# Performance work log

Measured on AMD Instinct MI355X. Metric: run time of the kernel, lower is better.

The kernel has to match this reference:

```python
import math
import jax, jax.numpy as jnp
import numpy as np

D_IN, R_S, T_MAX = 1024, 256, 2048
B, T = 8, 2048


def setup_inputs() -> dict:
    key = jax.random.key(0)
    ks = jax.random.split(key, 8)
    u = jax.random.normal(ks[0], (B, T, D_IN), dtype=jnp.float32)
    h0_r = jax.random.normal(ks[1], (B, R_S), dtype=jnp.float32)
    h0_i = jax.random.normal(ks[2], (B, R_S), dtype=jnp.float32)
    # parameters (lambda_raw randomized instead of zeros so sigmoid is nontrivial)
    lambda_raw = jax.random.normal(ks[3], (R_S,), dtype=jnp.float32)
    # omega init exactly as in the torch module
    log_min, log_max = math.log(1.0 / T_MAX), math.log(math.pi)
    n = np.arange(1, R_S + 1, dtype=np.float32)
    weyl_freqs = n * math.pi / R_S
    log_freqs = np.exp(np.linspace(log_min, log_max, R_S, dtype=np.float32))
    omega = jnp.asarray(0.5 * weyl_freqs + 0.5 * log_freqs, dtype=jnp.float32)
    W_proj = jax.random.normal(ks[4], (R_S, D_IN), dtype=jnp.float32) / math.sqrt(D_IN)
    W_res = jax.random.normal(ks[5], (2 * R_S, D_IN), dtype=jnp.float32) / math.sqrt(D_IN)
    ln_gamma = jnp.ones((2 * R_S,), dtype=jnp.float32)
    ln_beta = jnp.zeros((2 * R_S,), dtype=jnp.float32)
    return {"u": u, "h0_r": h0_r, "h0_i": h0_i, "lambda_raw": lambda_raw,
            "omega": omega, "W_proj": W_proj, "W_res": W_res,
            "ln_gamma": ln_gamma, "ln_beta": ln_beta}


def _layernorm(x, gamma, beta, eps=1e-5):
    mu = jnp.mean(x, axis=-1, keepdims=True)
    var = jnp.mean(jnp.square(x - mu), axis=-1, keepdims=True)
    return (x - mu) * jax.lax.rsqrt(var + eps) * gamma + beta


def reference(u, h0_r, h0_i, lambda_raw, omega, W_proj, W_res, ln_gamma, ln_beta):
    Bb, Tt, _ = u.shape
    lam = -jax.nn.sigmoid(lambda_raw) * 5.0                      # [R]
    t = jnp.arange(Tt, dtype=jnp.float32)                        # [T]
    decay = jnp.exp(lam[:, None] * t[None, :])                   # [R,T]
    phase = omega[:, None] * t[None, :]                          # [R,T]
    f_r = decay * jnp.cos(phase)
    f_i = decay * jnp.sin(phase)
    u_proj = jnp.einsum('btd,rd->brt', u, W_proj)                # [B,R,T]
    n_fft = 2 * Tt
    U_f = jnp.fft.rfft(u_proj, n=n_fft, axis=-1)                 # [B,R,F]
    F_r = jnp.fft.rfft(f_r, n=n_fft, axis=-1)[None]              # [1,R,F]
    F_i = jnp.fft.rfft(f_i, n=n_fft, axis=-1)[None]
    h_r = jnp.fft.irfft(U_f * F_r, n=n_fft, axis=-1)[..., :Tt]   # [B,R,T]
    h_i = jnp.fft.irfft(U_f * F_i, n=n_fft, axis=-1)[..., :Tt]
    # ZIR correction from initial state
    t_zir = t + 1.0
    decay_z = jnp.exp(lam[:, None] * t_zir[None, :])             # [R,T]
    phase_z = omega[:, None] * t_zir[None, :]
    f_r_z = decay_z * jnp.cos(phase_z)
    f_i_z = decay_z * jnp.sin(phase_z)
    h0r = h0_r[:, :, None]                                       # [B,R,1]
    h0i = h0_i[:, :, None]
    h_r = h_r + h0r * f_r_z[None] - h0i * f_i_z[None]
    h_i = h_i + h0r * f_i_z[None] + h0i * f_r_z[None]
    h_r = jnp.swapaxes(h_r, 1, 2)                                # [B,T,R]
    h_i = jnp.swapaxes(h_i, 1, 2)
    ssm_out = jnp.concatenate([h_r, h_i], axis=-1)               # [B,T,2R]
    res = jnp.einsum('btd,ed->bte', u, W_res)                    # [B,T,2R]
    out = _layernorm(ssm_out + res, ln_gamma, ln_beta)
    final_r = jax.lax.stop_gradient(h_r[:, -1])
    final_i = jax.lax.stop_gradient(h_i[:, -1])
    return out, final_r, final_i
```

## Files before the change

### kernel.cpp

```cpp
#include <hip/hip_runtime.h>
#include <math.h>

#define T_LEN 2048
#define BB    8
#define RS    256
#define DIN   1024
#define NE    768
#define M_TOT (BB * T_LEN)
#define LCH   32
#define NCH   (T_LEN / LCH)
#define OUT_MAIN (M_TOT * 512)

typedef unsigned short ushort;
typedef unsigned int   uint;
typedef short  short8  __attribute__((ext_vector_type(8)));
typedef float  f32x4   __attribute__((ext_vector_type(4)));
typedef ushort ushort8 __attribute__((ext_vector_type(8)));

__device__ __forceinline__ ushort f2bf_rn(float x) {
    uint u = __float_as_uint(x);
    return (ushort)((u + 0x7FFFu + ((u >> 16) & 1u)) >> 16);
}
__device__ __forceinline__ float bf2f(ushort b) {
    return __uint_as_float(((uint)b) << 16);
}

__device__ __forceinline__ void gload16(const ushort* g, ushort* l) {
    __builtin_amdgcn_global_load_lds(
        (const __attribute__((address_space(1))) uint*)g,
        (__attribute__((address_space(3))) uint*)l, 16, 0, 0);
}

#define N8U  (M_TOT * DIN / 8)
#define N8WP (RS * DIN / 8)
#define N8WR (2 * RS * DIN / 8)
#define N8TOT (N8U + N8WP + N8WR)

__global__ __launch_bounds__(256) void split_kernel(
    const float* __restrict__ u, const float* __restrict__ wp,
    const float* __restrict__ wr, ushort* __restrict__ Uhi,
    ushort* __restrict__ Ulo, ushort* __restrict__ Whi, ushort* __restrict__ Wlo)
{
    const int i = blockIdx.x * 256 + threadIdx.x;
    if (i >= N8TOT) return;
    const float* src; ushort* hi; ushort* lo; int j;
    if (i < N8U)              { src = u;  hi = Uhi; lo = Ulo; j = i; }
    else if (i < N8U + N8WP)  { src = wp; hi = Whi; lo = Wlo; j = i - N8U; }
    else                      { src = wr; hi = Whi + (size_t)RS * DIN;
                                lo = Wlo + (size_t)RS * DIN; j = i - N8U - N8WP; }
    const float4 x0 = ((const float4*)src)[(size_t)j * 2 + 0];
    const float4 x1 = ((const float4*)src)[(size_t)j * 2 + 1];
    const float xs[8] = {x0.x, x0.y, x0.z, x0.w, x1.x, x1.y, x1.z, x1.w};
    ushort8 hv, lv;
#pragma unroll
    for (int k = 0; k < 8; ++k) {
        const ushort hb = f2bf_rn(xs[k]);
        hv[k] = hb;
        lv[k] = f2bf_rn(xs[k] - bf2f(hb));
    }
    ((ushort8*)hi)[j] = hv;
    ((ushort8*)lo)[j] = lv;
}

#define Bb 128
#define BK 32

__global__ __launch_bounds__(256) void gemm_mfma(
    const ushort* __restrict__ Uh, const ushort* __restrict__ Ul,
    const ushort* __restrict__ Wh, const ushort* __restrict__ Wl,
    float* __restrict__ C)
{
    __shared__ ushort Ah[Bb * BK], Al[Bb * BK], Bh[Bb * BK], Bl[Bb * BK];
    const int tid  = threadIdx.x;
    const int id   = blockIdx.x;
    const int sid  = (id & 7) * 96 + (id >> 3);
    const int bn   = sid % 6;
    const int bm   = sid / 6;
    const int wid  = tid >> 6;
    const int lane = tid & 63;
    const int wr   = wid >> 1, wc = wid & 1;
    const int fr   = lane & 15;
    const int fq   = lane >> 4;

    const int srow = tid >> 2;
    const int skk  = (tid & 3) * 8;
    const ushort* gAh = Uh + (size_t)(bm * 128 + srow) * DIN + skk;
    const ushort* gAl = Ul + (size_t)(bm * 128 + srow) * DIN + skk;
    const ushort* gBh = Wh + (size_t)(bn * 128 + srow) * DIN + skk;
    const ushort* gBl = Wl + (size_t)(bn * 128 + srow) * DIN + skk;
    ushort* lAh0 = Ah + tid * 8; ushort* lAh1 = Ah + 64 * BK + tid * 8;
    ushort* lAl0 = Al + tid * 8; ushort* lAl1 = Al + 64 * BK + tid * 8;
    ushort* lBh0 = Bh + tid * 8; ushort* lBh1 = Bh + 64 * BK + tid * 8;
    ushort* lBl0 = Bl + tid * 8; ushort* lBl1 = Bl + 64 * BK + tid * 8;
    const size_t rstep = (size_t)64 * DIN;

    f32x4 acc[4][4];
#pragma unroll
    for (int m = 0; m < 4; ++m)
#pragma unroll
        for (int n = 0; n < 4; ++n) acc[m][n] = (f32x4){0.f, 0.f, 0.f, 0.f};

    for (int kk = 0; kk < DIN; kk += BK) {
        gload16(gAh + kk, lAh0); gload16(gAh + kk + rstep, lAh1);
        gload16(gAl + kk, lAl0); gload16(gAl + kk + rstep, lAl1);
        gload16(gBh + kk, lBh0); gload16(gBh + kk + rstep, lBh1);
        gload16(gBl + kk, lBl0); gload16(gBl + kk + rstep, lBl1);
        __syncthreads();

        short8 ah[4], al[4], bh[4], bl[4];
#pragma unroll
        for (int m = 0; m < 4; ++m) {
            const int row = wr * 64 + m * 16 + fr;
            ah[m] = *(const short8*)&Ah[row * BK + fq * 8];
            al[m] = *(const short8*)&Al[row * BK + fq * 8];
        }
#pragma unroll
        for (int n = 0; n < 4; ++n) {
            const int col = wc * 64 + n * 16 + fr;
            bh[n] = *(const short8*)&Bh[col * BK + fq * 8];
            bl[n] = *(const short8*)&Bl[col * BK + fq * 8];
        }
#pragma unroll
        for (int m = 0; m < 4; ++m)
#pragma unroll
            for (int n = 0; n < 4; ++n) {
                acc[m][n] = __builtin_amdgcn_mfma_f32_16x16x32_bf16(ah[m], bh[n], acc[m][n], 0, 0, 0);
                acc[m][n] = __builtin_amdgcn_mfma_f32_16x16x32_bf16(ah[m], bl[n], acc[m][n], 0, 0, 0);
                acc[m][n] = __builtin_amdgcn_mfma_f32_16x16x32_bf16(al[m], bh[n], acc[m][n], 0, 0, 0);
            }
        __syncthreads();
    }

    const int crow0 = bm * 128 + wr * 64;
    const int ccol0 = bn * 128 + wc * 64;
#pragma unroll
    for (int m = 0; m < 4; ++m) {
        const int row = crow0 + m * 16 + fq * 4;
#pragma unroll
        for (int n = 0; n < 4; ++n) {
            const int col = ccol0 + n * 16 + fr;
#pragma unroll
            for (int j = 0; j < 4; ++j)
                C[(size_t)(row + j) * NE + col] = acc[m][n][j];
        }
    }
}

__device__ inline void pole(const float* __restrict__ lraw, const float* __restrict__ om,
                            int r, float& zr, float& zi, float& lam, float& o)
{
    const float x   = lraw[r];
    const float sig = 1.f / (1.f + expf(-x));
    lam = -5.f * sig;
    o   = om[r];
    const float er = expf(lam);
    zr = er * cosf(o);
    zi = er * sinf(o);
}

__global__ __launch_bounds__(256) void carry_kernel(
    const float* __restrict__ C, const float* __restrict__ lraw,
    const float* __restrict__ om, float2* __restrict__ carry)
{
    const int c = blockIdx.x, b = blockIdx.y, r = threadIdx.x;
    const int m0 = b * T_LEN + c * LCH;
    float zr, zi, lam, o;
    pole(lraw, om, r, zr, zi, lam, o);
    const float* p = C + (size_t)m0 * NE + r;
    float hr = 0.f, hi = 0.f;
#pragma unroll 8
    for (int s = 0; s < LCH; ++s) {
        const float u  = p[(size_t)s * NE];
        const float nr = zr * hr - zi * hi + u;
        const float ni = zr * hi + zi * hr;
        hr = nr; hi = ni;
    }
    carry[(size_t)(b * NCH + c) * RS + r] = make_float2(hr, hi);
}

__global__ __launch_bounds__(256) void scan_ln_kernel(
    const float* __restrict__ C, const float2* __restrict__ carry,
    const float* __restrict__ h0r, const float* __restrict__ h0i,
    const float* __restrict__ lraw, const float* __restrict__ om,
    const float* __restrict__ gamma, const float* __restrict__ beta,
    float* __restrict__ out)
{
    const int c = blockIdx.x, b = blockIdx.y, r = threadIdx.x;
    __shared__ float xt[8][512];
    const int m0 = b * T_LEN + c * LCH;
    float zr, zi, lam, o;
    pole(lraw, om, r, zr, zi, lam, o);

    const float eL  = expf(lam * (float)LCH);
    const float zLr = eL * cosf(o * (float)LCH);
    const float zLi = eL * sinf(o * (float)LCH);
    float ar = 0.f, ai = 0.f;
    const float2* cp = carry + (size_t)b * NCH * RS + r;
    for (int j = 0; j < c; ++j) {
        const float2 k = cp[(size_t)j * RS];
        const float nr = zLr * ar - zLi * ai + k.x;
        const float ni = zLr * ai + zLi * ar + k.y;
        ar = nr; ai = ni;
    }
    const float tL  = (float)(LCH * c);
    const float dz  = expf(lam * tL);
    const float pzr = dz * cosf(o * tL);
    const float pzi = dz * sinf(o * tL);
    const float h0R = h0r[b * RS + r];
    const float h0I = h0i[b * RS + r];
    float2 st;
    st.x = ar + h0R * pzr - h0I * pzi;
    st.y = ai + h0R * pzi + h0I * pzr;

    const int wid = r >> 6, lane = r & 63;
    const float4 g0  = *(const float4*)&gamma[lane * 8];
    const float4 g1  = *(const float4*)&gamma[lane * 8 + 4];
    const float4 be0 = *(const float4*)&beta[lane * 8];
    const float4 be1 = *(const float4*)&beta[lane * 8 + 4];

    for (int batch = 0; batch < 4; ++batch) {
        const int s0 = batch * 8;
#pragma unroll
        for (int s = 0; s < 8; ++s) {
            const int m = m0 + s0 + s;
            const float u  = C[(size_t)m * NE + r];
            const float hr = zr * st.x - zi * st.y + u;
            const float hi = zr * st.y + zi * st.x;
            st.x = hr; st.y = hi;
            xt[s][r]       = hr + C[(size_t)m * NE + 256 + r];
            xt[s][256 + r] = hi + C[(size_t)m * NE + 512 + r];
        }
        __syncthreads();
#pragma unroll
        for (int rr = 0; rr < 2; ++rr) {
            const int s = wid * 2 + rr;
            const int m = m0 + s0 + s;
            const float4 x0 = *(const float4*)&xt[s][lane * 8];
            const float4 x1 = *(const float4*)&xt[s][lane * 8 + 4];
            float s1 = (x0.x + x0.y) + (x0.z + x0.w) + (x1.x + x1.y) + (x1.z + x1.w);
            float s2 = (x0.x * x0.x + x0.y * x0.y) + (x0.z * x0.z + x0.w * x0.w)
                     + (x1.x * x1.x + x1.y * x1.y) + (x1.z * x1.z + x1.w * x1.w);
#pragma unroll
            for (int off = 1; off < 64; off <<= 1) {
                s1 += __shfl_xor(s1, off);
                s2 += __shfl_xor(s2, off);
            }
            const float mu   = s1 * (1.f / 512.f);
            const float var  = s2 * (1.f / 512.f) - mu * mu;
            const float rstd = rsqrtf(var + 1e-5f);
            float4 o0, o1;
            o0.x = (x0.x - mu) * rstd * g0.x + be0.x;
            o0.y = (x0.y - mu) * rstd * g0.y + be0.y;
            o0.z = (x0.z - mu) * rstd * g0.z + be0.z;
            o0.w = (x0.w - mu) * rstd * g0.w + be0.w;
            o1.x = (x1.x - mu) * rstd * g1.x + be1.x;
            o1.y = (x1.y - mu) * rstd * g1.y + be1.y;
            o1.z = (x1.z - mu) * rstd * g1.z + be1.z;
            o1.w = (x1.w - mu) * rstd * g1.w + be1.w;
            *(float4*)&out[(size_t)m * 512 + lane * 8]     = o0;
            *(float4*)&out[(size_t)m * 512 + lane * 8 + 4] = o1;
        }
        __syncthreads();
    }

    if (c == NCH - 1) {
        out[OUT_MAIN + b * RS + r]           = st.x;
        out[OUT_MAIN + BB * RS + b * RS + r] = st.y;
    }
}

extern "C" void kernel_launch(void* const* d_in, const int* in_sizes, int n_in,
                              void* d_out, int out_size, void* d_ws, size_t ws_size,
                              hipStream_t stream)
{
    const float* u    = (const float*)d_in[0];
    const float* h0r  = (const float*)d_in[1];
    const float* h0i  = (const float*)d_in[2];
    const float* lraw = (const float*)d_in[3];
    const float* omg  = (const float*)d_in[4];
    const float* Wp   = (const float*)d_in[5];
    const float* Wr   = (const float*)d_in[6];
    const float* gam  = (const float*)d_in[7];
    const float* bet  = (const float*)d_in[8];
    float* out = (float*)d_out;

    float*  C     = (float*)d_ws;
    float2* carry = (float2*)(C + (size_t)M_TOT * NE);
    ushort* Uhi   = (ushort*)(carry + (size_t)BB * NCH * RS);
    ushort* Ulo   = Uhi + (size_t)M_TOT * DIN;
    ushort* Whi   = Ulo + (size_t)M_TOT * DIN;
    ushort* Wlo   = Whi + (size_t)NE * DIN;

    split_kernel<<<N8TOT / 256, 256, 0, stream>>>(u, Wp, Wr, Uhi, Ulo, Whi, Wlo);
    gemm_mfma<<<768, 256, 0, stream>>>(Uhi, Ulo, Whi, Wlo, C);
    carry_kernel<<<dim3(NCH, BB), 256, 0, stream>>>(C, lraw, omg, carry);
    scan_ln_kernel<<<dim3(NCH, BB), 256, 0, stream>>>(C, (const float2*)carry,
                                                      h0r, h0i, lraw, omg, gam, bet, out);
}
```

Before: 227.0 us.

## Warp-specialize scan/LN kernel into scan and residual-loader halves

Blocks of scan_ln_kernel grow to 512 threads. The first 256 threads preload all 32 scan inputs into registers and compute the chunk prefix. That prefix is now a Horner-free weighted sum with 8-way batched carry loads instead of a serial recurrence, and it reuses the running power to replace the separate exp/cos/sin for h0. The other 256 threads load residual values as float2 and prefetch the next batch into registers while LayerNorm runs. Each of the 8 waves then normalizes one row per batch, which adds register pressure (uu[32]) and a second shared buffer.

Measured after the change: 227.6 us. No clear change (+0.3%).

```diff
diff --git a/kernel.cpp b/kernel.cpp
--- a/kernel.cpp
+++ b/kernel.cpp
@@ -178,65 +178,114 @@
     carry[(size_t)(b * NCH + c) * RS + r] = make_float2(hr, hi);
 }
 
-__global__ __launch_bounds__(256) void scan_ln_kernel(
+__global__ __launch_bounds__(512) void scan_ln_kernel(
     const float* __restrict__ C, const float2* __restrict__ carry,
     const float* __restrict__ h0r, const float* __restrict__ h0i,
     const float* __restrict__ lraw, const float* __restrict__ om,
     const float* __restrict__ gamma, const float* __restrict__ beta,
     float* __restrict__ out)
 {
-    const int c = blockIdx.x, b = blockIdx.y, r = threadIdx.x;
+    const int c = blockIdx.x, b = blockIdx.y, tid = threadIdx.x;
     __shared__ float xt[8][512];
-    const int m0 = b * T_LEN + c * LCH;
-    float zr, zi, lam, o;
-    pole(lraw, om, r, zr, zi, lam, o);
-
-    const float eL  = expf(lam * (float)LCH);
-    const float zLr = eL * cosf(o * (float)LCH);
-    const float zLi = eL * sinf(o * (float)LCH);
-    float ar = 0.f, ai = 0.f;
-    const float2* cp = carry + (size_t)b * NCH * RS + r;
-    for (int j = 0; j < c; ++j) {
-        const float2 k = cp[(size_t)j * RS];
-        const float nr = zLr * ar - zLi * ai + k.x;
-        const float ni = zLr * ai + zLi * ar + k.y;
-        ar = nr; ai = ni;
-    }
-    const float tL  = (float)(LCH * c);
-    const float dz  = expf(lam * tL);
-    const float pzr = dz * cosf(o * tL);
-    const float pzi = dz * sinf(o * tL);
-    const float h0R = h0r[b * RS + r];
-    const float h0I = h0i[b * RS + r];
-    float2 st;
-    st.x = ar + h0R * pzr - h0I * pzi;
-    st.y = ai + h0R * pzi + h0I * pzr;
-
-    const int wid = r >> 6, lane = r & 63;
+    __shared__ float rt[8][512];
+    const int m0   = b * T_LEN + c * LCH;
+    const int wid  = tid >> 6, lane = tid & 63;
+    const bool isScan = (tid < 256);
+    const int r    = tid & 255;
+
     const float4 g0  = *(const float4*)&gamma[lane * 8];
     const float4 g1  = *(const float4*)&gamma[lane * 8 + 4];
     const float4 be0 = *(const float4*)&beta[lane * 8];
     const float4 be1 = *(const float4*)&beta[lane * 8 + 4];
 
+    float   uu[32];
+    float2  st = make_float2(0.f, 0.f);
+    float   zr = 0.f, zi = 0.f;
+    float2  resreg[8];
+
+    if (isScan) {
+        const float* up = C + (size_t)m0 * NE + r;
+#pragma unroll
+        for (int s = 0; s < 32; ++s) uu[s] = up[(size_t)s * NE];
+
+        float lam, o;
+        pole(lraw, om, r, zr, zi, lam, o);
+        const float eL  = expf(lam * (float)LCH);
+        const float zLr = eL * cosf(o * (float)LCH);
+        const float zLi = eL * sinf(o * (float)LCH);
+
+        float ar = 0.f, ai = 0.f;
+        float wr_ = 1.f, wi_ = 0.f;
+        const float2* cp = carry + (size_t)b * NCH * RS + r;
+        int j = c - 1;
+        for (; j >= 7; j -= 8) {
+            float2 k[8];
+#pragma unroll
+            for (int t = 0; t < 8; ++t) k[t] = cp[(size_t)(j - t) * RS];
+#pragma unroll
+            for (int t = 0; t < 8; ++t) {
+                ar += wr_ * k[t].x - wi_ * k[t].y;
+                ai += wr_ * k[t].y + wi_ * k[t].x;
+                const float nwr = wr_ * zLr - wi_ * zLi;
+                const float nwi = wr_ * zLi + wi_ * zLr;
+                wr_ = nwr; wi_ = nwi;
+            }
+        }
+        for (; j >= 0; --j) {
+            const float2 k = cp[(size_t)j * RS];
+            ar += wr_ * k.x - wi_ * k.y;
+            ai += wr_ * k.y + wi_ * k.x;
+            const float nwr = wr_ * zLr - wi_ * zLi;
+            const float nwi = wr_ * zLi + wi_ * zLr;
+            wr_ = nwr; wi_ = nwi;
+        }
+        const float h0R = h0r[b * RS + r];
+        const float h0I = h0i[b * RS + r];
+        st.x = ar + h0R * wr_ - h0I * wi_;
+        st.y = ai + h0R * wi_ + h0I * wr_;
+    } else {
+        const float* rp = C + (size_t)m0 * NE + 256 + 2 * r;
+#pragma unroll
+        for (int s = 0; s < 8; ++s)
+            resreg[s] = *(const float2*)(rp + (size_t)s * NE);
+    }
+
+#pragma unroll
     for (int batch = 0; batch < 4; ++batch) {
-        const int s0 = batch * 8;
-#pragma unroll
-        for (int s = 0; s < 8; ++s) {
-            const int m = m0 + s0 + s;
-            const float u  = C[(size_t)m * NE + r];
-            const float hr = zr * st.x - zi * st.y + u;
-            const float hi = zr * st.y + zi * st.x;
-            st.x = hr; st.y = hi;
-            xt[s][r]       = hr + C[(size_t)m * NE + 256 + r];
-            xt[s][256 + r] = hi + C[(size_t)m * NE + 512 + r];
+        if (isScan) {
+#pragma unroll
+            for (int s = 0; s < 8; ++s) {
+                const float u  = uu[batch * 8 + s];
+                const float hr = zr * st.x - zi * st.y + u;
+                const float hi = zr * st.y + zi * st.x;
+                st.x = hr; st.y = hi;
+                xt[s][r]       = hr;
+                xt[s][256 + r] = hi;
+            }
+        } else {
+#pragma unroll
+            for (int s = 0; s < 8; ++s)
+                *(float2*)&rt[s][2 * r] = resreg[s];
         }
         __syncthreads();
-#pragma unroll
-        for (int rr = 0; rr < 2; ++rr) {
-            const int s = wid * 2 + rr;
-            const int m = m0 + s0 + s;
-            const float4 x0 = *(const float4*)&xt[s][lane * 8];
-            const float4 x1 = *(const float4*)&xt[s][lane * 8 + 4];
+
+        if (!isScan && batch < 3) {
+            const float* rp = C + (size_t)(m0 + (batch + 1) * 8) * NE + 256 + 2 * r;
+#pragma unroll
+            for (int s = 0; s < 8; ++s)
+                resreg[s] = *(const float2*)(rp + (size_t)s * NE);
+        }
+
+        {
+            const int s = wid;
+            const int m = m0 + batch * 8 + s;
+            const float4 ha = *(const float4*)&xt[s][lane * 8];
+            const float4 hb = *(const float4*)&xt[s][lane * 8 + 4];
+            const float4 ra = *(const float4*)&rt[s][lane * 8];
+            const float4 rb = *(const float4*)&rt[s][lane * 8 + 4];
+            float4 x0, x1;
+            x0.x = ha.x + ra.x; x0.y = ha.y + ra.y; x0.z = ha.z + ra.z; x0.w = ha.w + ra.w;
+            x1.x = hb.x + rb.x; x1.y = hb.y + rb.y; x1.z = hb.z + rb.z; x1.w = hb.w + rb.w;
             float s1 = (x0.x + x0.y) + (x0.z + x0.w) + (x1.x + x1.y) + (x1.z + x1.w);
             float s2 = (x0.x * x0.x + x0.y * x0.y) + (x0.z * x0.z + x0.w * x0.w)
                      + (x1.x * x1.x + x1.y * x1.y) + (x1.z * x1.z + x1.w * x1.w);
@@ -263,7 +312,7 @@
         __syncthreads();
     }
 
-    if (c == NCH - 1) {
+    if (c == NCH - 1 && isScan) {
         out[OUT_MAIN + b * RS + r]           = st.x;
         out[OUT_MAIN + BB * RS + b * RS + r] = st.y;
     }
@@ -294,6 +343,6 @@
     split_kernel<<<N8TOT / 256, 256, 0, stream>>>(u, Wp, Wr, Uhi, Ulo, Whi, Wlo);
     gemm_mfma<<<768, 256, 0, stream>>>(Uhi, Ulo, Whi, Wlo, C);
     carry_kernel<<<dim3(NCH, BB), 256, 0, stream>>>(C, lraw, omg, carry);
-    scan_ln_kernel<<<dim3(NCH, BB), 256, 0, stream>>>(C, (const float2*)carry,
+    scan_ln_kernel<<<dim3(NCH, BB), 512, 0, stream>>>(C, (const float2*)carry,
                                                       h0r, h0i, lraw, omg, gam, bet, out);
 }
```

## Fuse carry and scan kernels with decoupled lookback flags across chunk blocks

Applied to the files above, without the earlier changes.

Merges the chunk-carry kernel and the scan+layernorm kernel into one kernel. Each block keeps its chunk's inputs in registers, computes the local scan and publishes its carry through an atomic store plus a flag. It then waits for earlier chunks' flags and combines their carries, accumulating pole powers as it goes. This removes one launch and the second read of the C column, and replaces the closing exp/cos/sin power with the accumulated product. In exchange it relies on all 512 blocks being co-resident for the spin-wait, adds a memset launch, and raises register pressure from 64 held floats.

Result: slower. 274.3 us (+20.8%).

```diff
diff --git a/kernel.cpp b/kernel.cpp
--- a/kernel.cpp
+++ b/kernel.cpp
@@ -1,5 +1,6 @@
 #include <hip/hip_runtime.h>
 #include <math.h>
+#include <string.h>
 
 #define T_LEN 2048
 #define BB    8
@@ -13,6 +14,7 @@
 
 typedef unsigned short ushort;
 typedef unsigned int   uint;
+typedef unsigned long long u64;
 typedef short  short8  __attribute__((ext_vector_type(8)));
 typedef float  f32x4   __attribute__((ext_vector_type(4)));
 typedef ushort ushort8 __attribute__((ext_vector_type(8)));
@@ -158,28 +160,8 @@
     zi = er * sinf(o);
 }
 
-__global__ __launch_bounds__(256) void carry_kernel(
-    const float* __restrict__ C, const float* __restrict__ lraw,
-    const float* __restrict__ om, float2* __restrict__ carry)
-{
-    const int c = blockIdx.x, b = blockIdx.y, r = threadIdx.x;
-    const int m0 = b * T_LEN + c * LCH;
-    float zr, zi, lam, o;
-    pole(lraw, om, r, zr, zi, lam, o);
-    const float* p = C + (size_t)m0 * NE + r;
-    float hr = 0.f, hi = 0.f;
-#pragma unroll 8
-    for (int s = 0; s < LCH; ++s) {
-        const float u  = p[(size_t)s * NE];
-        const float nr = zr * hr - zi * hi + u;
-        const float ni = zr * hi + zi * hr;
-        hr = nr; hi = ni;
-    }
-    carry[(size_t)(b * NCH + c) * RS + r] = make_float2(hr, hi);
-}
-
-__global__ __launch_bounds__(256) void scan_ln_kernel(
-    const float* __restrict__ C, const float2* __restrict__ carry,
+__global__ __launch_bounds__(256, 4) void fused_scan_ln(
+    const float* __restrict__ C, u64* __restrict__ carry, int* __restrict__ flags,
     const float* __restrict__ h0r, const float* __restrict__ h0i,
     const float* __restrict__ lraw, const float* __restrict__ om,
     const float* __restrict__ gamma, const float* __restrict__ beta,
@@ -191,26 +173,101 @@
     float zr, zi, lam, o;
     pole(lraw, om, r, zr, zi, lam, o);
 
+    float ur[32], ui[32];
+    {
+        const float* up = C + (size_t)m0 * NE + r;
+#pragma unroll
+        for (int s = 0; s < 32; ++s) ur[s] = up[(size_t)s * NE];
+    }
+
+    {
+        float hr = 0.f, hi = 0.f;
+#pragma unroll
+        for (int s = 0; s < 32; ++s) {
+            const float nr = zr * hr - zi * hi + ur[s];
+            const float ni = zr * hi + zi * hr;
+            hr = nr; hi = ni;
+            ur[s] = hr; ui[s] = hi;
+        }
+    }
+
+    if (c < NCH - 1) {
+        float2 cv2 = make_float2(ur[31], ui[31]);
+        u64 cv; memcpy(&cv, &cv2, 8);
+        __hip_atomic_store(carry + ((size_t)b * NCH + c) * RS + r, cv,
+                           __ATOMIC_RELAXED, __HIP_MEMORY_SCOPE_AGENT);
+        __threadfence();
+        __syncthreads();
+        if (r == 0)
+            __hip_atomic_store(&flags[b * NCH + c], 1,
+                               __ATOMIC_RELEASE, __HIP_MEMORY_SCOPE_AGENT);
+    }
+
+    if (r < c) {
+        while (__hip_atomic_load(&flags[b * NCH + r], __ATOMIC_RELAXED,
+                                 __HIP_MEMORY_SCOPE_AGENT) == 0)
+            __builtin_amdgcn_s_sleep(4);
+        (void)__hip_atomic_load(&flags[b * NCH + r], __ATOMIC_ACQUIRE,
+                                __HIP_MEMORY_SCOPE_AGENT);
+    }
+    __syncthreads();
+
     const float eL  = expf(lam * (float)LCH);
     const float zLr = eL * cosf(o * (float)LCH);
     const float zLi = eL * sinf(o * (float)LCH);
     float ar = 0.f, ai = 0.f;
-    const float2* cp = carry + (size_t)b * NCH * RS + r;
-    for (int j = 0; j < c; ++j) {
-        const float2 k = cp[(size_t)j * RS];
-        const float nr = zLr * ar - zLi * ai + k.x;
-        const float ni = zLr * ai + zLi * ar + k.y;
-        ar = nr; ai = ni;
-    }
-    const float tL  = (float)(LCH * c);
-    const float dz  = expf(lam * tL);
-    const float pzr = dz * cosf(o * tL);
-    const float pzi = dz * sinf(o * tL);
+    float wr_ = 1.f, wi_ = 0.f;
+    {
+        const u64* cp = carry + (size_t)b * NCH * RS + r;
+        int j = c - 1;
+        for (; j >= 7; j -= 8) {
+            u64 kv[8];
+#pragma unroll
+            for (int t = 0; t < 8; ++t)
+                kv[t] = __hip_atomic_load(cp + (size_t)(j - t) * RS,
+                                          __ATOMIC_RELAXED, __HIP_MEMORY_SCOPE_AGENT);
+#pragma unroll
+            for (int t = 0; t < 8; ++t) {
+                float2 k; memcpy(&k, &kv[t], 8);
+                ar += wr_ * k.x - wi_ * k.y;
+                ai += wr_ * k.y + wi_ * k.x;
+                const float nwr = wr_ * zLr - wi_ * zLi;
+                const float nwi = wr_ * zLi + wi_ * zLr;
+                wr_ = nwr; wi_ = nwi;
+            }
+        }
+        for (; j >= 0; --j) {
+            u64 kv = __hip_atomic_load(cp + (size_t)j * RS,
+                                       __ATOMIC_RELAXED, __HIP_MEMORY_SCOPE_AGENT);
+            float2 k; memcpy(&k, &kv, 8);
+            ar += wr_ * k.x - wi_ * k.y;
+            ai += wr_ * k.y + wi_ * k.x;
+            const float nwr = wr_ * zLr - wi_ * zLi;
+            const float nwi = wr_ * zLi + wi_ * zLr;
+            wr_ = nwr; wi_ = nwi;
+        }
+    }
     const float h0R = h0r[b * RS + r];
     const float h0I = h0i[b * RS + r];
-    float2 st;
-    st.x = ar + h0R * pzr - h0I * pzi;
-    st.y = ai + h0R * pzi + h0I * pzr;
+    const float Sr = ar + h0R * wr_ - h0I * wi_;
+    const float Si = ai + h0R * wi_ + h0I * wr_;
+
+    {
+        float pr = zr * Sr - zi * Si;
+        float pi = zr * Si + zi * Sr;
+#pragma unroll
+        for (int t = 0; t < 32; ++t) {
+            ur[t] += pr; ui[t] += pi;
+            const float nr = pr * zr - pi * zi;
+            const float ni = pr * zi + pi * zr;
+            pr = nr; pi = ni;
+        }
+    }
+
+    if (c == NCH - 1) {
+        out[OUT_MAIN + b * RS + r]           = ur[31];
+        out[OUT_MAIN + BB * RS + b * RS + r] = ui[31];
+    }
 
     const int wid = r >> 6, lane = r & 63;
     const float4 g0  = *(const float4*)&gamma[lane * 8];
@@ -218,17 +275,14 @@
     const float4 be0 = *(const float4*)&beta[lane * 8];
     const float4 be1 = *(const float4*)&beta[lane * 8 + 4];
 
+#pragma unroll
     for (int batch = 0; batch < 4; ++batch) {
         const int s0 = batch * 8;
 #pragma unroll
         for (int s = 0; s < 8; ++s) {
             const int m = m0 + s0 + s;
-            const float u  = C[(size_t)m * NE + r];
-            const float hr = zr * st.x - zi * st.y + u;
-            const float hi = zr * st.y + zi * st.x;
-            st.x = hr; st.y = hi;
-            xt[s][r]       = hr + C[(size_t)m * NE + 256 + r];
-            xt[s][256 + r] = hi + C[(size_t)m * NE + 512 + r];
+            xt[s][r]       = ur[s0 + s] + C[(size_t)m * NE + 256 + r];
+            xt[s][256 + r] = ui[s0 + s] + C[(size_t)m * NE + 512 + r];
         }
         __syncthreads();
 #pragma unroll
@@ -262,11 +316,6 @@
         }
         __syncthreads();
     }
-
-    if (c == NCH - 1) {
-        out[OUT_MAIN + b * RS + r]           = st.x;
-        out[OUT_MAIN + BB * RS + b * RS + r] = st.y;
-    }
 }
 
 extern "C" void kernel_launch(void* const* d_in, const int* in_sizes, int n_in,
@@ -284,16 +333,17 @@
     const float* bet  = (const float*)d_in[8];
     float* out = (float*)d_out;
 
-    float*  C     = (float*)d_ws;
-    float2* carry = (float2*)(C + (size_t)M_TOT * NE);
-    ushort* Uhi   = (ushort*)(carry + (size_t)BB * NCH * RS);
+    float* C      = (float*)d_ws;
+    u64*   carry  = (u64*)(C + (size_t)M_TOT * NE);
+    int*   flags  = (int*)(carry + (size_t)BB * NCH * RS);
+    ushort* Uhi   = (ushort*)(flags + BB * NCH);
     ushort* Ulo   = Uhi + (size_t)M_TOT * DIN;
     ushort* Whi   = Ulo + (size_t)M_TOT * DIN;
     ushort* Wlo   = Whi + (size_t)NE * DIN;
 
+    hipMemsetAsync(flags, 0, BB * NCH * sizeof(int), stream);
     split_kernel<<<N8TOT / 256, 256, 0, stream>>>(u, Wp, Wr, Uhi, Ulo, Whi, Wlo);
     gemm_mfma<<<768, 256, 0, stream>>>(Uhi, Ulo, Whi, Wlo, C);
-    carry_kernel<<<dim3(NCH, BB), 256, 0, stream>>>(C, lraw, omg, carry);
-    scan_ln_kernel<<<dim3(NCH, BB), 256, 0, stream>>>(C, (const float2*)carry,
-                                                      h0r, h0i, lraw, omg, gam, bet, out);
-}
+    fused_scan_ln<<<dim3(NCH, BB), 256, 0, stream>>>(C, carry, flags,
+                                                     h0r, h0i, lraw, omg, gam, bet, out);
+}
```
